# Performance work log

Hardware: AMD Instinct MI355X
Metric: run time of the kernel (lower is better)

Reference implementation:

```python
import jax, jax.numpy as jnp
import numpy as np


def setup_inputs() -> dict:
    key = jax.random.key(0)
    k1, k2 = jax.random.split(key)
    N, P, T, H, W = 8, 32, 16, 384, 384
    # binary {0,1} masks, stored as float32 (original binarizes via bool().long())
    groups_pred = jax.random.randint(k1, (N, P, H, W), 0, 2).astype(jnp.float32)
    groups_true = jax.random.randint(k2, (N, T, H, W), 0, 2).astype(jnp.float32)
    return {"groups_pred": groups_pred, "groups_true": groups_true}


def reference(groups_pred, groups_true):
    # Binarize (matches .bool().long() in the original)
    Gp = (groups_pred != 0).astype(jnp.float32)  # (N,P,H,W)
    Gt = (groups_true != 0).astype(jnp.float32)  # (N,T,H,W)

    # Pairwise intersection as a batched contraction over H,W --
    # avoids materializing the (N,P,T,H,W) broadcast tensor.
    inter = jnp.einsum('nphw,nthw->npt', Gp, Gt)  # (N,P,T)

    # For binary masks: |Gp ∪ Gt| = |Gp| + |Gt| - |Gp ∩ Gt|
    area_p = Gp.sum(axis=(-2, -1))  # (N,P)
    area_t = Gt.sum(axis=(-2, -1))  # (N,T)
    union = area_p[:, :, None] + area_t[:, None, :] - inter  # (N,P,T)

    # ious with 0/0 -> 0 (original sets non-finite entries to 0)
    safe_union = jnp.where(union > 0, union, 1.0)
    ious = jnp.where(union > 0, inter / safe_union, 0.0)  # (N,P,T)

    iou_max = ious.max(axis=-1)  # (N,P): best-matching true segment per pred

    # Weighted per-pixel sum of best-IoU over predicted masks, normalized by coverage
    num = jnp.einsum('np,nphw->nhw', iou_max, Gp)  # (N,H,W)
    den = Gp.sum(axis=1)                            # (N,H,W)
    score = jnp.where(den > 0, num / jnp.where(den > 0, den, 1.0), 0.0)
    return score
```

## Files before the change

kernel.cpp:

```cpp
#include <hip/hip_runtime.h>
#include <cstdint>
#include <cstddef>

typedef unsigned long long u64;

constexpr int N_  = 8;
constexpr int P_  = 32;
constexpr int T_  = 16;
constexpr int HW  = 384 * 384;
constexpr int WORDS = HW / 64;
constexpr int GPN = HW / 256;
constexpr int PG  = N_ * P_ * HW / 256;
constexpr int TG  = N_ * T_ * HW / 256;
constexpr int TOTG = PG + TG;
constexpr int BATCH = 8;
constexpr int PACK_BLOCKS = 1728;

__global__ __launch_bounds__(256)
void pack_all(const float* __restrict__ gp, const float* __restrict__ gt,
              u64* __restrict__ pk) {
    const int lane = threadIdx.x & 63;
    const int wave = blockIdx.x * 4 + (threadIdx.x >> 6);

    #pragma unroll
    for (int it = 0; it < 4; ++it) {
        const int g0 = (wave * 4 + it) * BATCH;
        const float4* src = (g0 < PG)
            ? reinterpret_cast<const float4*>(gp) + (size_t)g0 * 64
            : reinterpret_cast<const float4*>(gt) + (size_t)(g0 - PG) * 64;

        float4 v[BATCH];
        #pragma unroll
        for (int i = 0; i < BATCH; ++i) v[i] = src[(size_t)i * 64 + lane];

        u64 w[BATCH][4];
        #pragma unroll
        for (int i = 0; i < BATCH; ++i) {
            w[i][0] = __ballot(v[i].x != 0.0f);
            w[i][1] = __ballot(v[i].y != 0.0f);
            w[i][2] = __ballot(v[i].z != 0.0f);
            w[i][3] = __ballot(v[i].w != 0.0f);
        }

        if (lane == 0) {
            ulonglong2* dst = reinterpret_cast<ulonglong2*>(pk + (size_t)g0 * 4);
            #pragma unroll
            for (int i = 0; i < BATCH; ++i) {
                ulonglong2 lo, hi;
                lo.x = w[i][0]; lo.y = w[i][1];
                hi.x = w[i][2]; hi.y = w[i][3];
                dst[2 * i]     = lo;
                dst[2 * i + 1] = hi;
            }
        }
    }
}

__global__ __launch_bounds__(256)
void ioumax_kernel(const u64* __restrict__ pp, const u64* __restrict__ pt,
                   float* __restrict__ ioumax) {
    __shared__ int   red[4][33];
    __shared__ int   tot[33];
    __shared__ float shiou[T_];

    const int np  = blockIdx.x;
    const int n   = np >> 5;
    const int tid = threadIdx.x;
    const int lane = tid & 63;
    const int wv   = tid >> 6;

    const u64* pw = pp + (size_t)np * WORDS;
    const u64* tb = pt + (size_t)n * T_ * WORDS;

    u64 a[9];
    #pragma unroll
    for (int k = 0; k < 9; ++k) a[k] = pw[tid + 256 * k];

    int ap = 0;
    int inter[T_] = {};
    int areat[T_] = {};
    for (int k = 0; k < 9; ++k) {
        u64 tw[T_];
        #pragma unroll
        for (int t = 0; t < T_; ++t) tw[t] = tb[(size_t)t * WORDS + tid + 256 * k];
        ap += __popcll(a[k]);
        #pragma unroll
        for (int t = 0; t < T_; ++t) {
            inter[t] += __popcll(a[k] & tw[t]);
            areat[t] += __popcll(tw[t]);
        }
    }

    int vals[33];
    vals[0] = ap;
    #pragma unroll
    for (int t = 0; t < T_; ++t) { vals[1 + t] = inter[t]; vals[1 + T_ + t] = areat[t]; }

    #pragma unroll
    for (int i = 0; i < 33; ++i) {
        int v = vals[i];
        v += __shfl_down(v, 32);
        v += __shfl_down(v, 16);
        v += __shfl_down(v, 8);
        v += __shfl_down(v, 4);
        v += __shfl_down(v, 2);
        v += __shfl_down(v, 1);
        if (lane == 0) red[wv][i] = v;
    }
    __syncthreads();
    if (tid < 33) tot[tid] = red[0][tid] + red[1][tid] + red[2][tid] + red[3][tid];
    __syncthreads();
    if (tid < T_) {
        float it = (float)tot[1 + tid];
        float u  = (float)tot[0] + (float)tot[1 + T_ + tid] - it;
        shiou[tid] = (u > 0.0f) ? it / u : 0.0f;
    }
    __syncthreads();
    if (tid == 0) {
        float best = 0.0f;
        #pragma unroll
        for (int t = 0; t < T_; ++t) best = fmaxf(best, shiou[t]);
        ioumax[np] = best;
    }
}

__global__ __launch_bounds__(256)
void score_kernel(const u64* __restrict__ pm,
                  const float* __restrict__ ioumax,
                  float* __restrict__ out) {
    __shared__ u64   wlds[P_][16];
    __shared__ float iou[P_];

    const int tid  = threadIdx.x;
    const int lane = tid & 63;
    const int wv   = tid >> 6;
    const int gblk = blockIdx.x * 4;
    const int n    = gblk / GPN;
    const int gl0  = gblk - n * GPN;

    {
        int p = tid >> 3, k = tid & 7;
        const u64* s = pm + (size_t)(n * P_ + p) * WORDS + (size_t)gl0 * 4 + 2 * k;
        *reinterpret_cast<ulonglong2*>(&wlds[p][2 * k]) =
            *reinterpret_cast<const ulonglong2*>(s);
    }
    if (tid < P_) iou[tid] = ioumax[n * P_ + tid];
    __syncthreads();

    float num0 = 0.f, num1 = 0.f, num2 = 0.f, num3 = 0.f;
    int   den0 = 0, den1 = 0, den2 = 0, den3 = 0;
    #pragma unroll
    for (int p = 0; p < P_; ++p) {
        float w8 = iou[p];
        u64 w0 = wlds[p][wv * 4 + 0];
        u64 w1 = wlds[p][wv * 4 + 1];
        u64 w2 = wlds[p][wv * 4 + 2];
        u64 w3 = wlds[p][wv * 4 + 3];
        unsigned b0 = (unsigned)(w0 >> lane) & 1u;
        unsigned b1 = (unsigned)(w1 >> lane) & 1u;
        unsigned b2 = (unsigned)(w2 >> lane) & 1u;
        unsigned b3 = (unsigned)(w3 >> lane) & 1u;
        num0 += b0 ? w8 : 0.0f;  den0 += b0;
        num1 += b1 ? w8 : 0.0f;  den1 += b1;
        num2 += b2 ? w8 : 0.0f;  den2 += b2;
        num3 += b3 ? w8 : 0.0f;  den3 += b3;
    }

    float4 o;
    o.x = den0 ? num0 / (float)den0 : 0.0f;
    o.y = den1 ? num1 / (float)den1 : 0.0f;
    o.z = den2 ? num2 / (float)den2 : 0.0f;
    o.w = den3 ? num3 / (float)den3 : 0.0f;
    reinterpret_cast<float4*>(out)[(size_t)(gblk + wv) * 64 + lane] = o;
}

extern "C" void kernel_launch(void* const* d_in, const int* in_sizes, int n_in,
                              void* d_out, int out_size, void* d_ws, size_t ws_size,
                              hipStream_t stream) {
    const float* gp = (const float*)d_in[0];
    const float* gt = (const float*)d_in[1];
    float* out = (float*)d_out;

    char* ws = (char*)d_ws;
    u64* packed   = (u64*)ws;
    u64* packed_p = packed;
    u64* packed_t = packed + (size_t)PG * 4;
    float* ioumax = (float*)(ws + (size_t)TOTG * 4 * 8);

    hipLaunchKernelGGL(pack_all, dim3(PACK_BLOCKS), dim3(256), 0, stream,
                       gp, gt, packed);
    hipLaunchKernelGGL(ioumax_kernel, dim3(N_ * P_), dim3(256), 0, stream,
                       packed_p, packed_t, ioumax);
    hipLaunchKernelGGL(score_kernel, dim3(N_ * GPN / 4), dim3(256), 0, stream,
                       packed_p, ioumax, out);
}
```

Before: 71.43 us.

## Pack bits per-thread with contiguous 64-float reads instead of wave ballots

The packing kernel now has each thread read 64 consecutive floats as 16 uint4 loads and build one 64-bit word with integer nonzero tests, replacing the per-wave ballot scheme. Bit order is now pixel-contiguous inside each word, so the score kernel reads one word per lane and extracts a 4-bit nibble for its 4 output pixels. This removes ballot and lane-0 store serialization. In exchange, each thread's 256-byte strided reads are less coalesced across a wave. The integer test treats -0.0 as nonzero, which differs from the float compare.

```diff
diff --git a/kernel.cpp b/kernel.cpp
--- a/kernel.cpp
+++ b/kernel.cpp
@@ -10,50 +10,38 @@
 constexpr int HW  = 384 * 384;
 constexpr int WORDS = HW / 64;
 constexpr int GPN = HW / 256;
-constexpr int PG  = N_ * P_ * HW / 256;
-constexpr int TG  = N_ * T_ * HW / 256;
-constexpr int TOTG = PG + TG;
-constexpr int BATCH = 8;
-constexpr int PACK_BLOCKS = 1728;
+constexpr int PW  = N_ * P_ * WORDS;
+constexpr int TW  = PW + N_ * T_ * WORDS;
+constexpr int PACK_BLOCKS = TW / 256;
 
 __global__ __launch_bounds__(256)
 void pack_all(const float* __restrict__ gp, const float* __restrict__ gt,
               u64* __restrict__ pk) {
-    const int lane = threadIdx.x & 63;
-    const int wave = blockIdx.x * 4 + (threadIdx.x >> 6);
+    const int w = blockIdx.x * 256 + threadIdx.x;
+    const uint4* s = (w < PW)
+        ? reinterpret_cast<const uint4*>(gp) + (size_t)w * 16
+        : reinterpret_cast<const uint4*>(gt) + (size_t)(w - PW) * 16;
 
+    uint4 v[16];
     #pragma unroll
-    for (int it = 0; it < 4; ++it) {
-        const int g0 = (wave * 4 + it) * BATCH;
-        const float4* src = (g0 < PG)
-            ? reinterpret_cast<const float4*>(gp) + (size_t)g0 * 64
-            : reinterpret_cast<const float4*>(gt) + (size_t)(g0 - PG) * 64;
+    for (int k = 0; k < 16; ++k) v[k] = s[k];
 
-        float4 v[BATCH];
-        #pragma unroll
-        for (int i = 0; i < BATCH; ++i) v[i] = src[(size_t)i * 64 + lane];
-
-        u64 w[BATCH][4];
-        #pragma unroll
-        for (int i = 0; i < BATCH; ++i) {
-            w[i][0] = __ballot(v[i].x != 0.0f);
-            w[i][1] = __ballot(v[i].y != 0.0f);
-            w[i][2] = __ballot(v[i].z != 0.0f);
-            w[i][3] = __ballot(v[i].w != 0.0f);
-        }
-
-        if (lane == 0) {
-            ulonglong2* dst = reinterpret_cast<ulonglong2*>(pk + (size_t)g0 * 4);
-            #pragma unroll
-            for (int i = 0; i < BATCH; ++i) {
-                ulonglong2 lo, hi;
-                lo.x = w[i][0]; lo.y = w[i][1];
-                hi.x = w[i][2]; hi.y = w[i][3];
-                dst[2 * i]     = lo;
-                dst[2 * i + 1] = hi;
-            }
-        }
+    unsigned lo = 0, hi = 0;
+    #pragma unroll
+    for (int k = 0; k < 8; ++k) {
+        lo |= ((v[k].x | (0u - v[k].x)) >> 31) << (4 * k + 0);
+        lo |= ((v[k].y | (0u - v[k].y)) >> 31) << (4 * k + 1);
+        lo |= ((v[k].z | (0u - v[k].z)) >> 31) << (4 * k + 2);
+        lo |= ((v[k].w | (0u - v[k].w)) >> 31) << (4 * k + 3);
     }
+    #pragma unroll
+    for (int k = 0; k < 8; ++k) {
+        hi |= ((v[8 + k].x | (0u - v[8 + k].x)) >> 31) << (4 * k + 0);
+        hi |= ((v[8 + k].y | (0u - v[8 + k].y)) >> 31) << (4 * k + 1);
+        hi |= ((v[8 + k].z | (0u - v[8 + k].z)) >> 31) << (4 * k + 2);
+        hi |= ((v[8 + k].w | (0u - v[8 + k].w)) >> 31) << (4 * k + 3);
+    }
+    pk[w] = ((u64)hi << 32) | lo;
 }
 
 __global__ __launch_bounds__(256)
@@ -147,23 +135,19 @@
     if (tid < P_) iou[tid] = ioumax[n * P_ + tid];
     __syncthreads();
 
+    const int widx = wv * 4 + (lane >> 4);
+    const int sh   = (lane & 15) * 4;
+
     float num0 = 0.f, num1 = 0.f, num2 = 0.f, num3 = 0.f;
     int   den0 = 0, den1 = 0, den2 = 0, den3 = 0;
     #pragma unroll
     for (int p = 0; p < P_; ++p) {
         float w8 = iou[p];
-        u64 w0 = wlds[p][wv * 4 + 0];
-        u64 w1 = wlds[p][wv * 4 + 1];
-        u64 w2 = wlds[p][wv * 4 + 2];
-        u64 w3 = wlds[p][wv * 4 + 3];
-        unsigned b0 = (unsigned)(w0 >> lane) & 1u;
-        unsigned b1 = (unsigned)(w1 >> lane) & 1u;
-        unsigned b2 = (unsigned)(w2 >> lane) & 1u;
-        unsigned b3 = (unsigned)(w3 >> lane) & 1u;
-        num0 += b0 ? w8 : 0.0f;  den0 += b0;
-        num1 += b1 ? w8 : 0.0f;  den1 += b1;
-        num2 += b2 ? w8 : 0.0f;  den2 += b2;
-        num3 += b3 ? w8 : 0.0f;  den3 += b3;
+        unsigned nib = (unsigned)(wlds[p][widx] >> sh) & 0xFu;
+        num0 += (nib & 1u) ? w8 : 0.0f;  den0 += nib & 1u;
+        num1 += (nib & 2u) ? w8 : 0.0f;  den1 += (nib >> 1) & 1u;
+        num2 += (nib & 4u) ? w8 : 0.0f;  den2 += (nib >> 2) & 1u;
+        num3 += (nib & 8u) ? w8 : 0.0f;  den3 += (nib >> 3) & 1u;
     }
 
     float4 o;
@@ -184,8 +168,8 @@
     char* ws = (char*)d_ws;
     u64* packed   = (u64*)ws;
     u64* packed_p = packed;
-    u64* packed_t = packed + (size_t)PG * 4;
-    float* ioumax = (float*)(ws + (size_t)TOTG * 4 * 8);
+    u64* packed_t = packed + (size_t)PW;
+    float* ioumax = (float*)(ws + (size_t)TW * 8);
 
     hipLaunchKernelGGL(pack_all, dim3(PACK_BLOCKS), dim3(256), 0, stream,
                        gp, gt, packed);
```

New measurement: 80.96 us. +13.3%, slower.
